# Optimization experiments

Hardware: AMD Instinct MI355X
Metric: run time of the kernel (lower is better)

Reference implementation:

```python
import jax, jax.numpy as jnp
import numpy as np

N_NODES = 100000
N_EDGES = 1600000
IN_SIZE, HID_SIZE, OUT_SIZE = 128, 64, 64


def _glorot(key, shape):
    lim = float(np.sqrt(6.0 / (shape[0] + shape[1])))
    return jax.random.uniform(key, shape, jnp.float32, -lim, lim)


def setup_inputs() -> dict:
    key = jax.random.key(0)
    ks = jax.random.split(key, 6)
    features = jax.random.normal(ks[0], (N_NODES, IN_SIZE), jnp.float32)
    src = jax.random.randint(ks[1], (N_EDGES,), 0, N_NODES)
    dst = jax.random.randint(ks[2], (N_EDGES,), 0, N_NODES)
    return {
        "features": features,
        "W0": _glorot(ks[3], (IN_SIZE, HID_SIZE)),
        "b0": jnp.zeros((HID_SIZE,), jnp.float32),
        "W1": _glorot(ks[4], (HID_SIZE, HID_SIZE)),
        "b1": jnp.zeros((HID_SIZE,), jnp.float32),
        "W2": _glorot(ks[5], (HID_SIZE, OUT_SIZE)),
        "b2": jnp.zeros((OUT_SIZE,), jnp.float32),
        "src": src,
        "dst": dst,
    }


def reference(features, W0, b0, W1, b1, W2, b2, src, dst):
    # DGL GraphConv with norm='both': h' = relu(D_in^{-1/2} A D_out^{-1/2} h W + b)
    # Dropout layers are identity in eval mode (deterministic baseline).
    N = features.shape[0]
    ones = jnp.ones(src.shape, features.dtype)
    deg_out = jax.ops.segment_sum(ones, src, num_segments=N)
    deg_in = jax.ops.segment_sum(ones, dst, num_segments=N)
    norm_src = jnp.where(deg_out > 0, deg_out, 1.0) ** -0.5  # [N]
    norm_dst = jnp.where(deg_in > 0, deg_in, 1.0) ** -0.5    # [N]

    def layer(h, W, b):
        h = h * norm_src[:, None]          # source-side degree norm
        m = (h @ W)[src]                   # project first (in >= out), then gather [E, d_out]
        agg = jax.ops.segment_sum(m, dst, num_segments=N)  # scatter-add to destinations
        return jax.nn.relu(agg * norm_dst[:, None] + b)

    h = layer(features, W0, b0)
    h = layer(h, W1, b1)
    return layer(h, W2, b2)
```

## Files before the change

### kernel.cpp

```cpp
#include <hip/hip_runtime.h>
#include <hip/hip_bf16.h>

typedef __hip_bfloat16 bf16;
typedef __attribute__((ext_vector_type(8))) short bf16x8;
typedef __attribute__((ext_vector_type(8))) unsigned short u16x8;
typedef __attribute__((ext_vector_type(4))) float f32x4;
typedef __attribute__((ext_vector_type(4))) int i32x4;
typedef __attribute__((ext_vector_type(4))) short s16x4;

__device__ __forceinline__ float b2f(unsigned short u) {
  return __uint_as_float(((unsigned)u) << 16);
}
__device__ __forceinline__ unsigned short f2b(float x) {
  bf16 h = __float2bfloat16(x);
  return *reinterpret_cast<unsigned short*>(&h);
}

__global__ void k_passA(const int* __restrict__ src, const int* __restrict__ dst, int E,
                        int nbuck, int M, int* __restrict__ counts,
                        const unsigned short* __restrict__ raw, int* __restrict__ flag) {
  if (blockIdx.x == 256) {
    __shared__ int sbad, snz;
    const int t = threadIdx.x;
    if (t == 0) { sbad = 0; snz = 0; }
    __syncthreads();
    const unsigned short u = raw[t];
    const float a = fabsf(b2f(u));
    if (!(a < 100.f)) atomicAdd(&sbad, 1);
    if (((t & 1) == 0) && u != 0) atomicAdd(&snz, 1);
    __syncthreads();
    if (t == 0) flag[0] = (sbad == 0 && snz > 0) ? 1 : 0;
    return;
  }
  extern __shared__ int lh[];
  int* lh1 = lh;
  int* lh2 = lh + nbuck;
  const int t = threadIdx.x;
  for (int k = t; k < 2 * nbuck; k += 256) lh[k] = 0;
  __syncthreads();
  const int chunk = (E + 255) / 256;
  const int s = blockIdx.x * chunk;
  const int e = min(E, s + chunk);
  for (int i = s + t; i < e; i += 256) {
    atomicAdd(&lh1[dst[i] >> 8], 1);
    atomicAdd(&lh2[src[i] >> 8], 1);
  }
  __syncthreads();
  for (int k = t; k < nbuck; k += 256) {
    counts[k * 256 + blockIdx.x] = lh1[k];
    counts[M + k * 256 + blockIdx.x] = lh2[k];
  }
}

__global__ void k_scan1(const int* __restrict__ a, int M2, int* __restrict__ bsums) {
  __shared__ int sdata[256];
  int i = blockIdx.x * 256 + threadIdx.x;
  int v = (i < M2) ? a[i] : 0;
  sdata[threadIdx.x] = v;
  __syncthreads();
  for (int s = 128; s > 0; s >>= 1) {
    if (threadIdx.x < s) sdata[threadIdx.x] += sdata[threadIdx.x + s];
    __syncthreads();
  }
  if (threadIdx.x == 0) bsums[blockIdx.x] = sdata[0];
}

__global__ void k_scan2(int* __restrict__ bsums, int nb, int* __restrict__ rowStart,
                        int N, int E) {
  __shared__ int s[1024];
  const int t = threadIdx.x;
  const int v = (t < nb) ? bsums[t] : 0;
  s[t] = v;
  __syncthreads();
  for (int off = 1; off < 1024; off <<= 1) {
    int u = (t >= off) ? s[t - off] : 0;
    __syncthreads();
    s[t] += u;
    __syncthreads();
  }
  if (t < nb) bsums[t] = s[t] - v;
  if (t == 0) rowStart[N] = E;
}

__global__ void k_scan3(int* __restrict__ a, int M2, const int* __restrict__ bsums) {
  __shared__ int sdata[256];
  int i = blockIdx.x * 256 + threadIdx.x;
  int v = (i < M2) ? a[i] : 0;
  sdata[threadIdx.x] = v;
  __syncthreads();
  for (int off = 1; off < 256; off <<= 1) {
    int t = (threadIdx.x >= off) ? sdata[threadIdx.x - off] : 0;
    __syncthreads();
    sdata[threadIdx.x] += t;
    __syncthreads();
  }
  if (i < M2) a[i] = bsums[blockIdx.x] + sdata[threadIdx.x] - v;
}

__global__ void k_passC(const int* __restrict__ src, const int* __restrict__ dst, int E,
                        int nbuck, int M, const int* __restrict__ S,
                        int* __restrict__ tmp, unsigned char* __restrict__ tmp2) {
  extern __shared__ int cur[];
  int* cur1 = cur;
  int* cur2 = cur + nbuck;
  const int t = threadIdx.x;
  for (int k = t; k < nbuck; k += 256) {
    cur1[k] = S[k * 256 + blockIdx.x];
    cur2[k] = S[M + k * 256 + blockIdx.x];
  }
  __syncthreads();
  const int chunk = (E + 255) / 256;
  const int s = blockIdx.x * chunk;
  const int e = min(E, s + chunk);
  for (int i = s + t; i < e; i += 256) {
    const int sv = src[i];
    const int d = dst[i];
    const int pos1 = atomicAdd(&cur1[d >> 8], 1);
    tmp[pos1] = sv | ((d & 255) << 20);
    const int pos2 = atomicAdd(&cur2[sv >> 8], 1);
    tmp2[pos2 - E] = (unsigned char)(sv & 255);
  }
}

__global__ void k_passD(const int* __restrict__ tmp, const unsigned char* __restrict__ tmp2,
                        const int* __restrict__ S, int nbuck, int M, int N, int E,
                        int* __restrict__ rowStart, int* __restrict__ edgeSrc,
                        float* __restrict__ ns, float* __restrict__ nd) {
  __shared__ int h[256];
  __shared__ int ex[256];
  __shared__ int c[256];
  const int t = threadIdx.x;
  const int k = blockIdx.x;
  const int node = k * 256 + t;
  const int bs2 = S[M + k * 256] - E;
  const int be2 = (k + 1 < nbuck) ? (S[M + (k + 1) * 256] - E) : E;
  h[t] = 0;
  __syncthreads();
  for (int i = bs2 + t; i < be2; i += 256) atomicAdd(&h[tmp2[i]], 1);
  __syncthreads();
  if (node < N) {
    int dov = h[t];
    if (dov <= 0) dov = 1;
    ns[node] = rsqrtf((float)dov);
  }
  __syncthreads();
  const int bs = S[k * 256];
  const int be = (k + 1 < nbuck) ? S[(k + 1) * 256] : E;
  h[t] = 0;
  __syncthreads();
  for (int i = bs + t; i < be; i += 256) atomicAdd(&h[tmp[i] >> 20], 1);
  __syncthreads();
  const int cnt = h[t];
  ex[t] = cnt;
  __syncthreads();
  for (int off = 1; off < 256; off <<= 1) {
    int u = (t >= off) ? ex[t - off] : 0;
    __syncthreads();
    ex[t] += u;
    __syncthreads();
  }
  const int excl = ex[t] - cnt;
  if (node < N) {
    rowStart[node] = bs + excl;
    nd[node] = rsqrtf((float)(cnt > 0 ? cnt : 1));
  }
  c[t] = bs + excl;
  __syncthreads();
  for (int i = bs + t; i < be; i += 256) {
    const int v = tmp[i];
    const int pos = atomicAdd(&c[v >> 20], 1);
    edgeSrc[pos] = v & 0xFFFFF;
  }
}

template <int K, bool FIRST, bool SCALE>
__device__ __forceinline__ void gemm_loadA(const void* hin, bool isb, int rowA,
                                           int quad, bf16x8* A) {
  constexpr int KT = K / 32;
  if (FIRST && !isb) {
    const float* hp = (const float*)hin + (size_t)rowA * K;
#pragma unroll
    for (int kt = 0; kt < KT; ++kt) {
      const float4 u0 = *(const float4*)(hp + kt * 32 + quad * 8);
      const float4 u1 = *(const float4*)(hp + kt * 32 + quad * 8 + 4);
      A[kt][0] = (short)f2b(u0.x); A[kt][1] = (short)f2b(u0.y);
      A[kt][2] = (short)f2b(u0.z); A[kt][3] = (short)f2b(u0.w);
      A[kt][4] = (short)f2b(u1.x); A[kt][5] = (short)f2b(u1.y);
      A[kt][6] = (short)f2b(u1.z); A[kt][7] = (short)f2b(u1.w);
    }
  } else {
    const unsigned short* hp = (const unsigned short*)hin + (size_t)rowA * K;
#pragma unroll
    for (int kt = 0; kt < KT; ++kt)
      A[kt] = *(const bf16x8*)(hp + kt * 32 + quad * 8);
  }
}

template <int K, bool FIRST, bool SCALE>
__global__ void __launch_bounds__(256) k_gemm(
    const void* __restrict__ hin, const void* __restrict__ Wv,
    const int* __restrict__ flag, const float* __restrict__ norm_src,
    int N, unsigned short* __restrict__ out) {
  constexpr int KT = K / 32;
  constexpr int ST = K + 8;
  constexpr int CST = 72;
  __shared__ unsigned short Wl[64 * ST];
  __shared__ unsigned short Cl[4][16 * CST];
  const bool isb = (*flag != 0);
  const int tid = threadIdx.x;

  {
    const unsigned short* Wus = (const unsigned short*)Wv;
    const float* Wf = (const float*)Wv;
    for (int i0 = tid * 8; i0 < K * 64; i0 += 2048) {
      const int k = i0 >> 6;
      const int n0 = i0 & 63;
      unsigned short v[8];
      if (isb) {
        const u16x8 u = *(const u16x8*)(Wus + i0);
#pragma unroll
        for (int j = 0; j < 8; ++j) v[j] = u[j];
      } else {
        const float4 f0 = *(const float4*)(Wf + i0);
        const float4 f1 = *(const float4*)(Wf + i0 + 4);
        v[0] = f2b(f0.x); v[1] = f2b(f0.y); v[2] = f2b(f0.z); v[3] = f2b(f0.w);
        v[4] = f2b(f1.x); v[5] = f2b(f1.y); v[6] = f2b(f1.z); v[7] = f2b(f1.w);
      }
#pragma unroll
      for (int j = 0; j < 8; ++j) Wl[(n0 + j) * ST + k] = v[j];
    }
  }
  __syncthreads();

  const int lane = tid & 63;
  const int quad = lane >> 4;
  const int l16 = lane & 15;
  const int w = tid >> 6;
  unsigned short* myC = &Cl[w][0];

  const int wid = blockIdx.x * 4 + w;
  const int nw = gridDim.x * 4;
  const int G = (N + 15) >> 4;

  bf16x8 A0[KT], A1[KT];
  if (wid < G) {
    int r0 = (wid << 4) + l16;
    if (r0 >= N) r0 = N - 1;
    gemm_loadA<K, FIRST, SCALE>(hin, isb, r0, quad, A0);
  }
  for (int g = wid; g < G; g += nw) {
    if (g + nw < G) {
      int r1 = ((g + nw) << 4) + l16;
      if (r1 >= N) r1 = N - 1;
      gemm_loadA<K, FIRST, SCALE>(hin, isb, r1, quad, A1);
    }
    f32x4 acc[4] = {{0.f, 0.f, 0.f, 0.f}, {0.f, 0.f, 0.f, 0.f},
                    {0.f, 0.f, 0.f, 0.f}, {0.f, 0.f, 0.f, 0.f}};
#pragma unroll
    for (int kt = 0; kt < KT; ++kt) {
      const int koff = kt * 32 + quad * 8;
#pragma unroll
      for (int nt = 0; nt < 4; ++nt) {
        const bf16x8 Bf = *(const bf16x8*)&Wl[(nt * 16 + l16) * ST + koff];
        acc[nt] = __builtin_amdgcn_mfma_f32_16x16x32_bf16(A0[kt], Bf, acc[nt], 0, 0, 0);
      }
    }
    const int rowD = quad * 4;
#pragma unroll
    for (int r = 0; r < 4; ++r) {
      const int nodeW = (g << 4) + rowD + r;
      const float f = (SCALE && nodeW < N) ? norm_src[nodeW] : 1.0f;
#pragma unroll
      for (int nt = 0; nt < 4; ++nt)
        myC[(rowD + r) * CST + nt * 16 + l16] = f2b(SCALE ? acc[nt][r] * f : acc[nt][r]);
    }
    const int row2 = lane >> 2;
    const int c0 = (lane & 3) * 16;
    const int node = (g << 4) + row2;
    if (node < N) {
      const u16x8 v0 = *(const u16x8*)&myC[row2 * CST + c0];
      const u16x8 v1 = *(const u16x8*)&myC[row2 * CST + c0 + 8];
      *(u16x8*)(out + (size_t)node * 64 + c0) = v0;
      *(u16x8*)(out + (size_t)node * 64 + c0 + 8) = v1;
    }
#pragma unroll
    for (int kt = 0; kt < KT; ++kt) A0[kt] = A1[kt];
  }
}

__device__ __forceinline__ void agg_chunk_compute(unsigned trbase, int cb32, int lo,
                                                  unsigned span, int quad, f32x4* acc) {
  const int posbase = cb32 + (quad << 2);
  const unsigned u0 = (unsigned)(posbase - lo);
  bf16x8 Af;
#pragma unroll
  for (int j = 0; j < 8; ++j) {
    const unsigned off = (j < 4) ? (unsigned)j : (unsigned)(12 + j);
    Af[j] = ((u0 + off) < span) ? (short)0x3F80 : (short)0;
  }
  s16x4 t0[4], t1[4];
#pragma unroll
  for (int nt = 0; nt < 4; ++nt) {
    const unsigned a = trbase + (unsigned)(nt * 1024);
    asm volatile("ds_read_b64_tr_b16 %0, %1" : "=v"(t0[nt]) : "v"(a) : "memory");
    asm volatile("ds_read_b64_tr_b16 %0, %1 offset:512" : "=v"(t1[nt]) : "v"(a) : "memory");
  }
  asm volatile("s_waitcnt lgkmcnt(0)" ::: "memory");
  __builtin_amdgcn_sched_barrier(0);
#pragma unroll
  for (int nt = 0; nt < 4; ++nt) {
    bf16x8 Bf;
    Bf[0] = t0[nt][0]; Bf[1] = t0[nt][1]; Bf[2] = t0[nt][2]; Bf[3] = t0[nt][3];
    Bf[4] = t1[nt][0]; Bf[5] = t1[nt][1]; Bf[6] = t1[nt][2]; Bf[7] = t1[nt][3];
    acc[nt] = __builtin_amdgcn_mfma_f32_16x16x32_bf16(Af, Bf, acc[nt], 0, 0, 0);
  }
}

template <bool LAST>
__global__ void __launch_bounds__(256) k_aggregate(
    const unsigned short* __restrict__ proj,
    const int* __restrict__ edgeSrc, const int* __restrict__ rowStart,
    const float* __restrict__ norm_dst, const float* __restrict__ norm_src,
    const void* __restrict__ bias, const int* __restrict__ flag,
    int N, int E, void* __restrict__ outp) {
  __shared__ unsigned short lds[4][2048];
  const bool isb = (*flag != 0);
  const int tid = threadIdx.x;
  const int w = tid >> 6;
  const int lane = tid & 63;
  const int l16 = lane & 15;
  const int quad = lane >> 4;
  const int e32 = lane & 31;
  const int p = lane >> 5;

  const int wid = blockIdx.x * 4 + w;
  const int g0 = wid * 8;

  float bcol[4];
#pragma unroll
  for (int nt = 0; nt < 4; ++nt) {
    const int col = nt * 16 + l16;
    bcol[nt] = isb ? b2f(((const unsigned short*)bias)[col]) : ((const float*)bias)[col];
  }

  const int cb = rowStart[min(g0, N)];
  const int ce = rowStart[min(g0 + 8, N)];
  const int L = ce - cb;
  const int nch = (L + 31) >> 5;

  const int rsi = min(g0 + min(l16, 8), N);
  const int rsj = min(g0 + min(l16 + 1, 8), N);
  const int lo = rowStart[rsi];
  const unsigned span = (unsigned)(rowStart[rsj] - lo);

  int idxc[6];
#pragma unroll
  for (int t = 0; t < 6; ++t) {
    const int pos = min(cb + t * 32 + e32, E - 1);
    idxc[t] = edgeSrc[pos];
  }

  unsigned short* myl = &lds[w][0];
  unsigned wofs[4];
#pragma unroll
  for (int q = 0; q < 4; ++q) {
    const int n0 = p * 32 + q * 8;
    wofs[q] = (unsigned)((n0 >> 4) * 512 + e32 * 16 + (n0 & 15));
  }
  const unsigned trbase = (unsigned)(uintptr_t)myl + (unsigned)lane * 8u;

  f32x4 acc[4] = {{0.f, 0.f, 0.f, 0.f}, {0.f, 0.f, 0.f, 0.f},
                  {0.f, 0.f, 0.f, 0.f}, {0.f, 0.f, 0.f, 0.f}};

  i32x4 gb[2][4];
#define AGG_ISSUE(t, b)                                                         \
  {                                                                             \
    const unsigned short* rp = proj + (size_t)idxc[t] * 64 + p * 32;            \
    gb[b][0] = *(const i32x4*)(rp);                                             \
    gb[b][1] = *(const i32x4*)(rp + 8);                                         \
    gb[b][2] = *(const i32x4*)(rp + 16);                                        \
    gb[b][3] = *(const i32x4*)(rp + 24);                                        \
  }
  if (0 < nch) AGG_ISSUE(0, 0);
  if (1 < nch) AGG_ISSUE(1, 1);

#pragma unroll
  for (int tt = 0; tt < 6; ++tt) {
    if (tt < nch) {
#pragma unroll
      for (int q = 0; q < 4; ++q) *(i32x4*)(myl + wofs[q]) = gb[tt & 1][q];
      if (tt + 2 < 6 && tt + 2 < nch) AGG_ISSUE(tt + 2, tt & 1);
      asm volatile("s_waitcnt lgkmcnt(0)" ::: "memory");
      agg_chunk_compute(trbase, cb + tt * 32, lo, span, quad, acc);
    }
  }
  for (int t = 6; t < nch; ++t) {
    const int pos = min(cb + t * 32 + e32, E - 1);
    const int idx = edgeSrc[pos];
    const unsigned short* rp = proj + (size_t)idx * 64 + p * 32;
    i32x4 g4[4];
    g4[0] = *(const i32x4*)(rp);
    g4[1] = *(const i32x4*)(rp + 8);
    g4[2] = *(const i32x4*)(rp + 16);
    g4[3] = *(const i32x4*)(rp + 24);
#pragma unroll
    for (int q = 0; q < 4; ++q) *(i32x4*)(myl + wofs[q]) = g4[q];
    asm volatile("s_waitcnt lgkmcnt(0)" ::: "memory");
    agg_chunk_compute(trbase, cb + t * 32, lo, span, quad, acc);
  }
#undef AGG_ISSUE

  if (LAST && !isb) {
    float* fs = (float*)myl;
#pragma unroll
    for (int reg = 0; reg < 4; ++reg) {
      const int row = quad * 4 + reg;
      if (row < 8) {
        const int node = min(g0 + row, N - 1);
        const float nd = norm_dst[node];
#pragma unroll
        for (int nt = 0; nt < 4; ++nt)
          fs[row * 64 + nt * 16 + l16] = fmaxf(fmaf(acc[nt][reg], nd, bcol[nt]), 0.f);
      }
    }
    asm volatile("s_waitcnt lgkmcnt(0)" ::: "memory");
    __builtin_amdgcn_sched_barrier(0);
    const int r = lane >> 3;
    const int c0 = (lane & 7) * 8;
    const int node = g0 + r;
    if (node < N) {
      const float4 v0 = *(const float4*)&fs[r * 64 + c0];
      const float4 v1 = *(const float4*)&fs[r * 64 + c0 + 4];
      float* of = (float*)outp + (size_t)node * 64 + c0;
      *(float4*)of = v0;
      *(float4*)(of + 4) = v1;
    }
  } else {
#pragma unroll
    for (int reg = 0; reg < 4; ++reg) {
      const int row = quad * 4 + reg;
      if (row < 8) {
        const int node = min(g0 + row, N - 1);
        const float nd = norm_dst[node];
        const float esc = LAST ? 1.f : norm_src[node];
#pragma unroll
        for (int nt = 0; nt < 4; ++nt) {
          float x = fmaxf(fmaf(acc[nt][reg], nd, bcol[nt]), 0.f);
          if (!LAST) x *= esc;
          myl[row * 64 + nt * 16 + l16] = f2b(x);
        }
      }
    }
    asm volatile("s_waitcnt lgkmcnt(0)" ::: "memory");
    __builtin_amdgcn_sched_barrier(0);
    if (lane < 32) {
      const int r = lane >> 2;
      const int c0 = (lane & 3) * 16;
      const int node = g0 + r;
      if (node < N) {
        const u16x8 v0 = *(const u16x8*)&myl[r * 64 + c0];
        const u16x8 v1 = *(const u16x8*)&myl[r * 64 + c0 + 8];
        *(u16x8*)((unsigned short*)outp + (size_t)node * 64 + c0) = v0;
        *(u16x8*)((unsigned short*)outp + (size_t)node * 64 + c0 + 8) = v1;
      }
    }
  }
}

extern "C" void kernel_launch(void* const* d_in, const int* in_sizes, int n_in,
                              void* d_out, int out_size, void* d_ws, size_t ws_size,
                              hipStream_t stream) {
  const void* features = d_in[0];
  const void* W0 = d_in[1];
  const void* b0 = d_in[2];
  const void* W1 = d_in[3];
  const void* b1 = d_in[4];
  const void* W2 = d_in[5];
  const void* b2 = d_in[6];
  const int* src = (const int*)d_in[7];
  const int* dst = (const int*)d_in[8];
  const int N = in_sizes[0] / 128;
  const int E = in_sizes[7];
  const int NBUCK = (N + 255) >> 8;
  const int M = NBUCK * 256;
  const int M2 = 2 * M;

  char* w = (char*)d_ws;
  size_t off = 0;
  auto alloc = [&](size_t bytes) {
    void* p = w + off;
    off = (off + bytes + 255) & ~(size_t)255;
    return p;
  };
  int* flag = (int*)alloc(4);
  int* rowStart = (int*)alloc((size_t)(N + 1) * 4);
  int* counts = (int*)alloc((size_t)M2 * 4);
  int* bsums = (int*)alloc(1024 * 4);
  float* norm_src = (float*)alloc((size_t)N * 4);
  float* norm_dst = (float*)alloc((size_t)N * 4);
  int* tmp = (int*)alloc((size_t)E * 4);
  unsigned char* tmp2 = (unsigned char*)alloc((size_t)E);
  int* edgeSrc = (int*)alloc((size_t)E * 4);
  unsigned short* projA = (unsigned short*)alloc((size_t)N * 64 * 2);
  unsigned short* hB = (unsigned short*)d_out;

  const size_t lds_nb = (size_t)NBUCK * 2 * 4;
  const int G16 = (N + 15) / 16;
  const int GB = (G16 + 7) / 8;

  k_passA<<<257, 256, lds_nb, stream>>>(src, dst, E, NBUCK, M, counts,
                                        (const unsigned short*)features, flag);
  const int NB2 = (M2 + 255) / 256;
  k_scan1<<<NB2, 256, 0, stream>>>(counts, M2, bsums);
  k_scan2<<<1, 1024, 0, stream>>>(bsums, NB2, rowStart, N, E);
  k_scan3<<<NB2, 256, 0, stream>>>(counts, M2, bsums);
  k_passC<<<256, 256, lds_nb, stream>>>(src, dst, E, NBUCK, M, counts, tmp, tmp2);
  k_passD<<<NBUCK, 256, 0, stream>>>(tmp, tmp2, counts, NBUCK, M, N, E,
                                     rowStart, edgeSrc, norm_src, norm_dst);

  const int AB = (((N + 7) / 8) + 3) / 4;
  k_gemm<128, true, true><<<GB, 256, 0, stream>>>(features, W0, flag, norm_src, N, projA);
  k_aggregate<false><<<AB, 256, 0, stream>>>(projA, edgeSrc, rowStart, norm_dst, norm_src, b0, flag, N, E, hB);
  k_gemm<64, false, false><<<GB, 256, 0, stream>>>(hB, W1, flag, nullptr, N, projA);
  k_aggregate<false><<<AB, 256, 0, stream>>>(projA, edgeSrc, rowStart, norm_dst, norm_src, b1, flag, N, E, hB);
  k_gemm<64, false, false><<<GB, 256, 0, stream>>>(hB, W2, flag, nullptr, N, projA);
  k_aggregate<true><<<AB, 256, 0, stream>>>(projA, edgeSrc, rowStart, norm_dst, norm_src, b2, flag, N, E, d_out);
}
```

Measured before the change: 315.4 us.

## Fuse next-layer projection GEMM into aggregation epilogue

```diff
diff --git a/kernel.cpp b/kernel.cpp
--- a/kernel.cpp
+++ b/kernel.cpp
@@ -316,13 +316,13 @@
   }
 }
 
-template <bool LAST>
+template <bool LAST, bool FUSE>
 __global__ void __launch_bounds__(256) k_aggregate(
     const unsigned short* __restrict__ proj,
     const int* __restrict__ edgeSrc, const int* __restrict__ rowStart,
     const float* __restrict__ norm_dst, const float* __restrict__ norm_src,
     const void* __restrict__ bias, const int* __restrict__ flag,
-    int N, int E, void* __restrict__ outp) {
+    const void* __restrict__ Wv, int N, int E, void* __restrict__ outp) {
   __shared__ unsigned short lds[4][2048];
   const bool isb = (*flag != 0);
   const int tid = threadIdx.x;
@@ -410,58 +410,130 @@
   }
 #undef AGG_ISSUE
 
-  if (LAST && !isb) {
-    float* fs = (float*)myl;
+  if constexpr (FUSE) {
+    __shared__ unsigned short hT[32 * 72];
+    __shared__ unsigned short Wl2[64 * 72];
+    {
+      const unsigned short* Wus = (const unsigned short*)Wv;
+      const float* Wf = (const float*)Wv;
+      for (int i0 = tid * 8; i0 < 64 * 64; i0 += 2048) {
+        const int k = i0 >> 6;
+        const int n0 = i0 & 63;
+        unsigned short v[8];
+        if (isb) {
+          const u16x8 u = *(const u16x8*)(Wus + i0);
+#pragma unroll
+          for (int j = 0; j < 8; ++j) v[j] = u[j];
+        } else {
+          const float4 f0 = *(const float4*)(Wf + i0);
+          const float4 f1 = *(const float4*)(Wf + i0 + 4);
+          v[0] = f2b(f0.x); v[1] = f2b(f0.y); v[2] = f2b(f0.z); v[3] = f2b(f0.w);
+          v[4] = f2b(f1.x); v[5] = f2b(f1.y); v[6] = f2b(f1.z); v[7] = f2b(f1.w);
+        }
+#pragma unroll
+        for (int j = 0; j < 8; ++j) Wl2[(n0 + j) * 72 + k] = v[j];
+      }
+    }
 #pragma unroll
     for (int reg = 0; reg < 4; ++reg) {
       const int row = quad * 4 + reg;
       if (row < 8) {
         const int node = min(g0 + row, N - 1);
         const float nd = norm_dst[node];
-#pragma unroll
-        for (int nt = 0; nt < 4; ++nt)
-          fs[row * 64 + nt * 16 + l16] = fmaxf(fmaf(acc[nt][reg], nd, bcol[nt]), 0.f);
-      }
-    }
-    asm volatile("s_waitcnt lgkmcnt(0)" ::: "memory");
-    __builtin_amdgcn_sched_barrier(0);
-    const int r = lane >> 3;
-    const int c0 = (lane & 7) * 8;
-    const int node = g0 + r;
+        const float esc = norm_src[node];
+#pragma unroll
+        for (int nt = 0; nt < 4; ++nt) {
+          const float x = fmaxf(fmaf(acc[nt][reg], nd, bcol[nt]), 0.f) * esc;
+          hT[(w * 8 + row) * 72 + nt * 16 + l16] = f2b(x);
+        }
+      }
+    }
+    __syncthreads();
+    const int r0 = (w & 1) * 16;
+    const int cb2 = (w >> 1) * 32;
+    bf16x8 Afr[2], Bfr[2][2];
+#pragma unroll
+    for (int kt = 0; kt < 2; ++kt) {
+      const int koff = kt * 32 + quad * 8;
+      Afr[kt] = *(const bf16x8*)&hT[(r0 + l16) * 72 + koff];
+#pragma unroll
+      for (int nt = 0; nt < 2; ++nt)
+        Bfr[kt][nt] = *(const bf16x8*)&Wl2[(cb2 + nt * 16 + l16) * 72 + koff];
+    }
+    f32x4 acc2[2] = {{0.f, 0.f, 0.f, 0.f}, {0.f, 0.f, 0.f, 0.f}};
+#pragma unroll
+    for (int kt = 0; kt < 2; ++kt)
+#pragma unroll
+      for (int nt = 0; nt < 2; ++nt)
+        acc2[nt] = __builtin_amdgcn_mfma_f32_16x16x32_bf16(Afr[kt], Bfr[kt][nt], acc2[nt], 0, 0, 0);
+    __syncthreads();
+#pragma unroll
+    for (int nt = 0; nt < 2; ++nt)
+#pragma unroll
+      for (int reg = 0; reg < 4; ++reg) {
+        const int row = r0 + quad * 4 + reg;
+        hT[row * 72 + cb2 + nt * 16 + l16] = f2b(acc2[nt][reg]);
+      }
+    __syncthreads();
+    const int row = tid >> 3;
+    const int c0 = (tid & 7) * 8;
+    const int node = blockIdx.x * 32 + row;
     if (node < N) {
-      const float4 v0 = *(const float4*)&fs[r * 64 + c0];
-      const float4 v1 = *(const float4*)&fs[r * 64 + c0 + 4];
-      float* of = (float*)outp + (size_t)node * 64 + c0;
-      *(float4*)of = v0;
-      *(float4*)(of + 4) = v1;
+      *(u16x8*)((unsigned short*)outp + (size_t)node * 64 + c0) =
+          *(const u16x8*)&hT[row * 72 + c0];
     }
   } else {
-#pragma unroll
-    for (int reg = 0; reg < 4; ++reg) {
-      const int row = quad * 4 + reg;
-      if (row < 8) {
-        const int node = min(g0 + row, N - 1);
-        const float nd = norm_dst[node];
-        const float esc = LAST ? 1.f : norm_src[node];
-#pragma unroll
-        for (int nt = 0; nt < 4; ++nt) {
-          float x = fmaxf(fmaf(acc[nt][reg], nd, bcol[nt]), 0.f);
-          if (!LAST) x *= esc;
-          myl[row * 64 + nt * 16 + l16] = f2b(x);
+    if (!isb) {
+      float* fs = (float*)myl;
+#pragma unroll
+      for (int reg = 0; reg < 4; ++reg) {
+        const int row = quad * 4 + reg;
+        if (row < 8) {
+          const int node = min(g0 + row, N - 1);
+          const float nd = norm_dst[node];
+#pragma unroll
+          for (int nt = 0; nt < 4; ++nt)
+            fs[row * 64 + nt * 16 + l16] = fmaxf(fmaf(acc[nt][reg], nd, bcol[nt]), 0.f);
         }
       }
-    }
-    asm volatile("s_waitcnt lgkmcnt(0)" ::: "memory");
-    __builtin_amdgcn_sched_barrier(0);
-    if (lane < 32) {
-      const int r = lane >> 2;
-      const int c0 = (lane & 3) * 16;
+      asm volatile("s_waitcnt lgkmcnt(0)" ::: "memory");
+      __builtin_amdgcn_sched_barrier(0);
+      const int r = lane >> 3;
+      const int c0 = (lane & 7) * 8;
       const int node = g0 + r;
       if (node < N) {
-        const u16x8 v0 = *(const u16x8*)&myl[r * 64 + c0];
-        const u16x8 v1 = *(const u16x8*)&myl[r * 64 + c0 + 8];
-        *(u16x8*)((unsigned short*)outp + (size_t)node * 64 + c0) = v0;
-        *(u16x8*)((unsigned short*)outp + (size_t)node * 64 + c0 + 8) = v1;
+        const float4 v0 = *(const float4*)&fs[r * 64 + c0];
+        const float4 v1 = *(const float4*)&fs[r * 64 + c0 + 4];
+        float* of = (float*)outp + (size_t)node * 64 + c0;
+        *(float4*)of = v0;
+        *(float4*)(of + 4) = v1;
+      }
+    } else {
+#pragma unroll
+      for (int reg = 0; reg < 4; ++reg) {
+        const int row = quad * 4 + reg;
+        if (row < 8) {
+          const int node = min(g0 + row, N - 1);
+          const float nd = norm_dst[node];
+#pragma unroll
+          for (int nt = 0; nt < 4; ++nt) {
+            const float x = fmaxf(fmaf(acc[nt][reg], nd, bcol[nt]), 0.f);
+            myl[row * 64 + nt * 16 + l16] = f2b(x);
+          }
+        }
+      }
+      asm volatile("s_waitcnt lgkmcnt(0)" ::: "memory");
+      __builtin_amdgcn_sched_barrier(0);
+      if (lane < 32) {
+        const int r = lane >> 2;
+        const int c0 = (lane & 3) * 16;
+        const int node = g0 + r;
+        if (node < N) {
+          const u16x8 v0 = *(const u16x8*)&myl[r * 64 + c0];
+          const u16x8 v1 = *(const u16x8*)&myl[r * 64 + c0 + 8];
+          *(u16x8*)((unsigned short*)outp + (size_t)node * 64 + c0) = v0;
+          *(u16x8*)((unsigned short*)outp + (size_t)node * 64 + c0 + 8) = v1;
+        }
       }
     }
   }
@@ -502,11 +574,10 @@
   unsigned char* tmp2 = (unsigned char*)alloc((size_t)E);
   int* edgeSrc = (int*)alloc((size_t)E * 4);
   unsigned short* projA = (unsigned short*)alloc((size_t)N * 64 * 2);
-  unsigned short* hB = (unsigned short*)d_out;
+  unsigned short* projB = (unsigned short*)alloc((size_t)N * 64 * 2);
 
   const size_t lds_nb = (size_t)NBUCK * 2 * 4;
-  const int G16 = (N + 15) / 16;
-  const int GB = (G16 + 7) / 8;
+  const int GB = 1024;
 
   k_passA<<<257, 256, lds_nb, stream>>>(src, dst, E, NBUCK, M, counts,
                                         (const unsigned short*)features, flag);
@@ -520,9 +591,10 @@
 
   const int AB = (((N + 7) / 8) + 3) / 4;
   k_gemm<128, true, true><<<GB, 256, 0, stream>>>(features, W0, flag, norm_src, N, projA);
-  k_aggregate<false><<<AB, 256, 0, stream>>>(projA, edgeSrc, rowStart, norm_dst, norm_src, b0, flag, N, E, hB);
-  k_gemm<64, false, false><<<GB, 256, 0, stream>>>(hB, W1, flag, nullptr, N, projA);
-  k_aggregate<false><<<AB, 256, 0, stream>>>(projA, edgeSrc, rowStart, norm_dst, norm_src, b1, flag, N, E, hB);
-  k_gemm<64, false, false><<<GB, 256, 0, stream>>>(hB, W2, flag, nullptr, N, projA);
-  k_aggregate<true><<<AB, 256, 0, stream>>>(projA, edgeSrc, rowStart, norm_dst, norm_src, b2, flag, N, E, d_out);
-}
+  k_aggregate<false, true><<<AB, 256, 0, stream>>>(projA, edgeSrc, rowStart, norm_dst,
+                                                   norm_src, b0, flag, W1, N, E, projB);
+  k_aggregate<false, true><<<AB, 256, 0, stream>>>(projB, edgeSrc, rowStart, norm_dst,
+                                                   norm_src, b1, flag, W2, N, E, projA);
+  k_aggregate<true, false><<<AB, 256, 0, stream>>>(projA, edgeSrc, rowStart, norm_dst,
+                                                   norm_src, b2, flag, nullptr, N, E, d_out);
+}
```

Result: faster. 300.2 us (-4.8%).
